# Optimization experiments

Hardware: AMD Instinct MI355X
Metric: run time of the kernel (lower is better)

## Reference

```python
import jax, jax.numpy as jnp
import numpy as np

MI_N, DIS_N = 16384, 8192
EM = 128
E_MM, E_DD = MI_N * 32, DIS_N * 32


def _add_self_loops(edges, ew, n):
    loop = jnp.arange(n, dtype=edges.dtype)
    row = jnp.concatenate([edges[0], loop])
    col = jnp.concatenate([edges[1], loop])
    ew = jnp.concatenate([ew, jnp.ones((n,), ew.dtype)])
    return row, col, ew


def gcn_conv(x, edges, w, b, n, ew=None):
    # PyG GCNConv: symmetric gcn_norm with self-loops (fill 1.0), then
    # out[col] += norm * (x @ w)[row], plus bias.
    if ew is None:
        ew = jnp.ones((edges.shape[1],), x.dtype)
    row, col, ew = _add_self_loops(edges, ew, n)
    deg = jax.ops.segment_sum(ew, col, num_segments=n)
    dinv = jnp.where(deg > 0, jax.lax.rsqrt(deg), 0.0)
    norm = dinv[row] * ew * dinv[col]          # [E+n]
    h = x @ w                                   # [n, d]
    return jax.ops.segment_sum(h[row] * norm[:, None], col, num_segments=n) + b


def gat_conv(x, edges, w, a_src, a_dst, b, n):
    # PyG GATConv, heads=1: per-edge attention LeakyReLU(0.2) + softmax over
    # incoming edges of each target node (self-loops added).
    h = x @ w                                   # [n, d]
    row, col, _ = _add_self_loops(edges, jnp.ones((edges.shape[1],), x.dtype), n)
    e = jax.nn.leaky_relu((h @ a_src)[row] + (h @ a_dst)[col], negative_slope=0.2)
    m = jax.ops.segment_max(e, col, num_segments=n)
    ex = jnp.exp(e - m[col])
    s = jax.ops.segment_sum(ex, col, num_segments=n)
    alpha = ex / s[col]                         # [E+n]
    return jax.ops.segment_sum(h[row] * alpha[:, None], col, num_segments=n) + b


def setup_inputs() -> dict:
    key = jax.random.key(0)
    ks = jax.random.split(key, 24)
    sc = 1.0 / np.sqrt(EM)
    d = {
        'mm_x0': jax.random.normal(ks[0], (MI_N, EM), jnp.float32),
        'dd_x0': jax.random.normal(ks[1], (DIS_N, EM), jnp.float32),
        'w1_mm': jax.random.normal(ks[2], (EM, EM), jnp.float32) * sc,
        'b1_mm': jnp.zeros((EM,), jnp.float32),
        'w2_mm': jax.random.normal(ks[3], (EM, EM), jnp.float32) * sc,
        'b2_mm': jnp.zeros((EM,), jnp.float32),
        'w3_mm': jax.random.normal(ks[4], (EM, EM), jnp.float32) * sc,
        'asrc_mm': jax.random.normal(ks[5], (EM,), jnp.float32) * sc,
        'adst_mm': jax.random.normal(ks[6], (EM,), jnp.float32) * sc,
        'b3_mm': jnp.zeros((EM,), jnp.float32),
        'w1_dd': jax.random.normal(ks[7], (EM, EM), jnp.float32) * sc,
        'b1_dd': jnp.zeros((EM,), jnp.float32),
        'w2_dd': jax.random.normal(ks[8], (EM, EM), jnp.float32) * sc,
        'b2_dd': jnp.zeros((EM,), jnp.float32),
        'w3_dd': jax.random.normal(ks[9], (EM, EM), jnp.float32) * sc,
        'asrc_dd': jax.random.normal(ks[10], (EM,), jnp.float32) * sc,
        'adst_dd': jax.random.normal(ks[11], (EM,), jnp.float32) * sc,
        'b3_dd': jnp.zeros((EM,), jnp.float32),
        'mm_ew': jax.random.uniform(ks[12], (E_MM,), jnp.float32),
        'dd_ew': jax.random.uniform(ks[13], (E_DD,), jnp.float32),
        'mm_edges': jax.random.randint(ks[14], (2, E_MM), 0, MI_N, jnp.int32),
        'dd_edges': jax.random.randint(ks[15], (2, E_DD), 0, DIS_N, jnp.int32),
    }
    return d


def reference(mm_x0, dd_x0, w1_mm, b1_mm, w2_mm, b2_mm, w3_mm, asrc_mm, adst_mm,
              b3_mm, w1_dd, b1_dd, w2_dd, b2_dd, w3_dd, asrc_dd, adst_dd, b3_dd,
              mm_ew, dd_ew, mm_edges, dd_edges):
    elu = jax.nn.elu
    m1 = elu(gcn_conv(mm_x0, mm_edges, w1_mm, b1_mm, MI_N, mm_ew))
    m2 = elu(gcn_conv(m1, mm_edges, w2_mm, b2_mm, MI_N))
    m3 = elu(gat_conv(m2, mm_edges, w3_mm, asrc_mm, adst_mm, b3_mm, MI_N))
    d1 = elu(gcn_conv(dd_x0, dd_edges, w1_dd, b1_dd, DIS_N, dd_ew))
    d2 = elu(gcn_conv(d1, dd_edges, w2_dd, b2_dd, DIS_N))
    d3 = elu(gat_conv(d2, dd_edges, w3_dd, asrc_dd, adst_dd, b3_dd, DIS_N))
    mi_fea = (m1 + m2 + m3) / 3.0
    dis_fea = (d1 + d2 + d3) / 3.0
    score_raw = mi_fea @ dis_fea.T              # [MI_N, DIS_N]
    mn, mx = jnp.min(score_raw), jnp.max(score_raw)
    denom = jnp.where(mx > mn, mx - mn, jnp.asarray(1.0, score_raw.dtype))
    score_norm = jnp.where(mx > mn, (score_raw - mn) / denom,
                           jnp.zeros_like(score_raw))
    score_norm = jnp.clip(score_norm, 0.0, 1.0)
    return score_norm, mi_fea, dis_fea
```

## Files before the change

### kernel.cpp

```cpp
#include <hip/hip_runtime.h>
#include <cstdint>
#include <cstddef>

#define MI_NN 16384
#define DIS_NN 8192
#define EMB 128
#define EMM (MI_NN*32)
#define EDD (DIS_NN*32)

typedef __attribute__((ext_vector_type(8))) short short8;
typedef __attribute__((ext_vector_type(4))) float f32x4;

__device__ __forceinline__ float leakyr(float x){ return x > 0.f ? x : 0.2f*x; }
__device__ __forceinline__ float eluf(float x){ return x > 0.f ? x : expm1f(x); }

__device__ __forceinline__ unsigned bf16u(float x){
  unsigned u = __float_as_uint(x);
  return (u + 0x7FFFu + ((u >> 16) & 1u)) >> 16;
}
__device__ __forceinline__ float bfl(unsigned p){ return __uint_as_float(p << 16); }
__device__ __forceinline__ float bfh(unsigned p){ return __uint_as_float(p & 0xFFFF0000u); }

__global__ __launch_bounds__(256) void k_count2g(const int* __restrict__ c0, int* __restrict__ n0c,
                                                 int E0, int nb0,
                                                 const int* __restrict__ c1, int* __restrict__ n1c,
                                                 int E1, unsigned* __restrict__ ctr){
  if (blockIdx.x == 0 && threadIdx.x == 0) ctr[0] = 0u;
  int b = blockIdx.x;
  const int* col; int* cnt; int E; int t;
  if (b < nb0){ col = c0; cnt = n0c; E = E0; t = b*256 + threadIdx.x; }
  else        { col = c1; cnt = n1c; E = E1; t = (b - nb0)*256 + threadIdx.x; }
  if (t < E) atomicAdd(&cnt[col[t]], 1);
}

__global__ __launch_bounds__(1024) void k_scan2g(const int* __restrict__ cnt0, int* __restrict__ rp0,
                                                 int n0, int E0,
                                                 const int* __restrict__ cnt1, int* __restrict__ rp1,
                                                 int n1, int E1){
  const int* cnt = blockIdx.x ? cnt1 : cnt0;
  int* rowptr    = blockIdx.x ? rp1  : rp0;
  int n          = blockIdx.x ? n1   : n0;
  int E          = blockIdx.x ? E1   : E0;
  __shared__ int lds[1024];
  int t = threadIdx.x;
  int chunk = n >> 10;
  int base = t*chunk;
  int s = 0;
  for (int i = 0; i < chunk; ++i) s += cnt[base+i];
  lds[t] = s; __syncthreads();
  for (int off = 1; off < 1024; off <<= 1){
    int v = (t >= off) ? lds[t-off] : 0;
    __syncthreads();
    lds[t] += v;
    __syncthreads();
  }
  int run = lds[t] - s;
  for (int i = 0; i < chunk; ++i){ rowptr[base+i] = run; run += cnt[base+i]; }
  if (t == 0) rowptr[n] = E;
}

__global__ __launch_bounds__(256) void k_fill2g(
    const int* __restrict__ r0a, const int* __restrict__ c0a, const float* __restrict__ w0a,
    const int* __restrict__ rp0, int* __restrict__ f0, int2* __restrict__ e0,
    int E0, int nb0,
    const int* __restrict__ r1a, const int* __restrict__ c1a, const float* __restrict__ w1a,
    const int* __restrict__ rp1, int* __restrict__ f1, int2* __restrict__ e1,
    int E1){
  int b = blockIdx.x;
  const int *row, *col; const float* ew; const int* rowptr;
  int* fill; int2* epk; int E, t;
  if (b < nb0){ row=r0a; col=c0a; ew=w0a; rowptr=rp0; fill=f0; epk=e0; E=E0; t=b*256+threadIdx.x; }
  else        { row=r1a; col=c1a; ew=w1a; rowptr=rp1; fill=f1; epk=e1; E=E1; t=(b-nb0)*256+threadIdx.x; }
  if (t < E){
    int c = col[t];
    int p = rowptr[c] + atomicAdd(&fill[c], 1);
    epk[p] = make_int2(row[t], __float_as_int(ew[t]));
  }
}

template<int FUSE>
__global__ __launch_bounds__(256) void k_gemm2g(
    const float* __restrict__ X0, const float* __restrict__ W0, ushort* __restrict__ H0, int nb0,
    const float* __restrict__ X1, const float* __restrict__ W1, ushort* __restrict__ H1,
    const float* __restrict__ as0, const float* __restrict__ ad0,
    float* __restrict__ es0, float* __restrict__ ed0,
    const float* __restrict__ as1, const float* __restrict__ ad1,
    float* __restrict__ es1, float* __restrict__ ed1){
  int b = blockIdx.x;
  const float *X, *W, *asr, *ads; ushort* H; float *es, *ed; int rb;
  if (b < nb0){ X=X0; W=W0; H=H0; asr=as0; ads=ad0; es=es0; ed=ed0; rb = b; }
  else        { X=X1; W=W1; H=H1; asr=as1; ads=ad1; es=es1; ed=ed1; rb = b - nb0; }
  __shared__ float wl[EMB*EMB];
  int t = threadIdx.x;
  {
    const float4* W4 = (const float4*)W;
    float4* L4 = (float4*)wl;
    #pragma unroll
    for (int i = 0; i < 16; ++i) L4[t + 256*i] = W4[t + 256*i];
  }
  __syncthreads();
  int jg = t & 31;
  int rg = t >> 5;
  int r0 = rb*32 + rg*4;
  f32x4 acc0 = {0,0,0,0}, acc1 = {0,0,0,0}, acc2 = {0,0,0,0}, acc3 = {0,0,0,0};
  const float4* X4 = (const float4*)X;
  for (int k4 = 0; k4 < 32; ++k4){
    float4 x0 = X4[(size_t)(r0+0)*32 + k4];
    float4 x1 = X4[(size_t)(r0+1)*32 + k4];
    float4 x2 = X4[(size_t)(r0+2)*32 + k4];
    float4 x3 = X4[(size_t)(r0+3)*32 + k4];
#define GSTEP(c0,c1,c2,c3,kq) { f32x4 w4 = *(const f32x4*)&wl[(kq)*EMB + jg*4]; \
      acc0 += (c0)*w4; acc1 += (c1)*w4; acc2 += (c2)*w4; acc3 += (c3)*w4; }
    GSTEP(x0.x, x1.x, x2.x, x3.x, k4*4+0)
    GSTEP(x0.y, x1.y, x2.y, x3.y, k4*4+1)
    GSTEP(x0.z, x1.z, x2.z, x3.z, k4*4+2)
    GSTEP(x0.w, x1.w, x2.w, x3.w, k4*4+3)
#undef GSTEP
  }
#define PACK2(o, a) { o.x = bf16u(a[0]) | (bf16u(a[1])<<16); o.y = bf16u(a[2]) | (bf16u(a[3])<<16); }
  uint2 o0, o1, o2, o3;
  PACK2(o0, acc0) PACK2(o1, acc1) PACK2(o2, acc2) PACK2(o3, acc3)
#undef PACK2
  ushort* out = H + (size_t)r0*EMB + jg*4;
  *(uint2*)(out)         = o0;
  *(uint2*)(out + EMB)   = o1;
  *(uint2*)(out + 2*EMB) = o2;
  *(uint2*)(out + 3*EMB) = o3;

  if (FUSE){
    f32x4 s4 = *(const f32x4*)&asr[jg*4];
    f32x4 d4 = *(const f32x4*)&ads[jg*4];
    float ps0 = acc0[0]*s4[0] + acc0[1]*s4[1] + acc0[2]*s4[2] + acc0[3]*s4[3];
    float ps1 = acc1[0]*s4[0] + acc1[1]*s4[1] + acc1[2]*s4[2] + acc1[3]*s4[3];
    float ps2 = acc2[0]*s4[0] + acc2[1]*s4[1] + acc2[2]*s4[2] + acc2[3]*s4[3];
    float ps3 = acc3[0]*s4[0] + acc3[1]*s4[1] + acc3[2]*s4[2] + acc3[3]*s4[3];
    float pd0 = acc0[0]*d4[0] + acc0[1]*d4[1] + acc0[2]*d4[2] + acc0[3]*d4[3];
    float pd1 = acc1[0]*d4[0] + acc1[1]*d4[1] + acc1[2]*d4[2] + acc1[3]*d4[3];
    float pd2 = acc2[0]*d4[0] + acc2[1]*d4[1] + acc2[2]*d4[2] + acc2[3]*d4[3];
    float pd3 = acc3[0]*d4[0] + acc3[1]*d4[1] + acc3[2]*d4[2] + acc3[3]*d4[3];
    #pragma unroll
    for (int off = 16; off; off >>= 1){
      ps0 += __shfl_xor(ps0, off); ps1 += __shfl_xor(ps1, off);
      ps2 += __shfl_xor(ps2, off); ps3 += __shfl_xor(ps3, off);
      pd0 += __shfl_xor(pd0, off); pd1 += __shfl_xor(pd1, off);
      pd2 += __shfl_xor(pd2, off); pd3 += __shfl_xor(pd3, off);
    }
    if (jg == 0){
      es[r0+0] = ps0; es[r0+1] = ps1; es[r0+2] = ps2; es[r0+3] = ps3;
      ed[r0+0] = pd0; ed[r0+1] = pd1; ed[r0+2] = pd2; ed[r0+3] = pd3;
    }
  }
}

__global__ __launch_bounds__(256) void k_deg2g(
    const int* __restrict__ rp0, const int2* __restrict__ ep0,
    float* __restrict__ d10, float* __restrict__ d20, int n0, int nb0,
    const int* __restrict__ rp1, const int2* __restrict__ ep1,
    float* __restrict__ d11, float* __restrict__ d21, int n1){
  int b = blockIdx.x;
  const int* rowptr; const int2* epk; float *d1, *d2; int n, wid;
  int lane = threadIdx.x & 63;
  if (b < nb0){ rowptr=rp0; epk=ep0; d1=d10; d2=d20; n=n0; wid = (b*256 + threadIdx.x) >> 6; }
  else        { rowptr=rp1; epk=ep1; d1=d11; d2=d21; n=n1; wid = ((b-nb0)*256 + threadIdx.x) >> 6; }
  if (wid >= n) return;
  int beg = rowptr[wid], end = rowptr[wid+1];
  float s = 0.f;
  for (int i = beg + lane; i < end; i += 64) s += __int_as_float(epk[i].y);
  #pragma unroll
  for (int off = 32; off; off >>= 1) s += __shfl_xor(s, off);
  if (lane == 0){
    d1[wid] = rsqrtf(1.0f + s);
    d2[wid] = rsqrtf(1.0f + (float)(end - beg));
  }
}

__global__ __launch_bounds__(256) void k_agg2g(
    const ushort* __restrict__ H0, const float* __restrict__ di0, const int* __restrict__ rp0,
    const int2* __restrict__ ep0, const float* __restrict__ bi0,
    float* __restrict__ xn0, float* __restrict__ fe0, int n0, int nb0,
    const ushort* __restrict__ H1, const float* __restrict__ di1, const int* __restrict__ rp1,
    const int2* __restrict__ ep1, const float* __restrict__ bi1,
    float* __restrict__ xn1, float* __restrict__ fe1, int n1,
    int useew, int femode){
  int b = blockIdx.x;
  const ushort* H; const float* dinv; const int* rowptr; const int2* epk;
  const float* bias; float* xnext; float* fea; int n, wid;
  int lane = threadIdx.x & 63;
  if (b < nb0){ H=H0; dinv=di0; rowptr=rp0; epk=ep0; bias=bi0; xnext=xn0; fea=fe0; n=n0;
                wid = (b*256 + threadIdx.x) >> 6; }
  else        { H=H1; dinv=di1; rowptr=rp1; epk=ep1; bias=bi1; xnext=xn1; fea=fe1; n=n1;
                wid = ((b-nb0)*256 + threadIdx.x) >> 6; }
  if (wid >= n) return;
  int v = wid;
  int half = lane >> 5;
  int hl   = lane & 31;
  float dv = dinv[v];
  uint2 hv = *(const uint2*)(H + (size_t)v*EMB + hl*4);
  float a0, a1, a2, a3;
  if (half == 0){
    a0 = dv*bfl(hv.x); a1 = dv*bfh(hv.x); a2 = dv*bfl(hv.y); a3 = dv*bfh(hv.y);
  } else { a0 = a1 = a2 = a3 = 0.f; }
  int beg = rowptr[v], end = rowptr[v+1];
  int i = beg + half;
  for (; i + 2 < end; i += 4){
    int2 eA = epk[i], eB = epk[i+2];
    float nA = dinv[eA.x], nB = dinv[eB.x];
    if (useew){ nA *= __int_as_float(eA.y); nB *= __int_as_float(eB.y); }
    uint2 hA = *(const uint2*)(H + (size_t)eA.x*EMB + hl*4);
    uint2 hB = *(const uint2*)(H + (size_t)eB.x*EMB + hl*4);
    a0 += nA*bfl(hA.x) + nB*bfl(hB.x);
    a1 += nA*bfh(hA.x) + nB*bfh(hB.x);
    a2 += nA*bfl(hA.y) + nB*bfl(hB.y);
    a3 += nA*bfh(hA.y) + nB*bfh(hB.y);
  }
  if (i < end){
    int2 e = epk[i];
    float nm = dinv[e.x];
    if (useew) nm *= __int_as_float(e.y);
    uint2 h = *(const uint2*)(H + (size_t)e.x*EMB + hl*4);
    a0 += nm*bfl(h.x); a1 += nm*bfh(h.x); a2 += nm*bfl(h.y); a3 += nm*bfh(h.y);
  }
  a0 += __shfl_xor(a0, 32); a1 += __shfl_xor(a1, 32);
  a2 += __shfl_xor(a2, 32); a3 += __shfl_xor(a3, 32);
  if (half == 0){
    float4 b4 = *(const float4*)(bias + hl*4);
    float o0 = eluf(dv*a0 + b4.x), o1 = eluf(dv*a1 + b4.y);
    float o2 = eluf(dv*a2 + b4.z), o3 = eluf(dv*a3 + b4.w);
    *(float4*)(xnext + (size_t)v*EMB + hl*4) = make_float4(o0, o1, o2, o3);
    float* fp = fea + (size_t)v*EMB + hl*4;
    if (femode == 0){
      *(float4*)fp = make_float4(o0, o1, o2, o3);
    } else {
      float4 f = *(float4*)fp;
      *(float4*)fp = make_float4(f.x + o0, f.y + o1, f.z + o2, f.w + o3);
    }
  }
}

__global__ __launch_bounds__(256) void k_gat2g(
    const ushort* __restrict__ H0, const float* __restrict__ es0, const float* __restrict__ ed0,
    const int* __restrict__ rp0, const int2* __restrict__ ep0, const float* __restrict__ bi0,
    float* __restrict__ fe0, unsigned* __restrict__ sh0, int n0, int nb0,
    const ushort* __restrict__ H1, const float* __restrict__ es1, const float* __restrict__ ed1,
    const int* __restrict__ rp1, const int2* __restrict__ ep1, const float* __restrict__ bi1,
    float* __restrict__ fe1, unsigned* __restrict__ sh1, int n1){
  int b = blockIdx.x;
  const ushort* H; const float *es, *ed; const int* rowptr; const int2* epk; const float* bias;
  float* fea; unsigned* shadow; int n, wid;
  int lane = threadIdx.x & 63;
  if (b < nb0){ H=H0; es=es0; ed=ed0; rowptr=rp0; epk=ep0; bias=bi0; fea=fe0; shadow=sh0; n=n0;
                wid = (b*256 + threadIdx.x) >> 6; }
  else        { H=H1; es=es1; ed=ed1; rowptr=rp1; epk=ep1; bias=bi1; fea=fe1; shadow=sh1; n=n1;
                wid = ((b-nb0)*256 + threadIdx.x) >> 6; }
  if (wid >= n) return;
  int v = wid;
  float edv = ed[v];
  float self_e = leakyr(es[v] + edv);
  int beg = rowptr[v], end = rowptr[v+1];
  float m = -3.4e38f, s = 0.f;
  for (int i = beg + lane; i < end; i += 64){
    float e = leakyr(es[epk[i].x] + edv);
    if (e > m){ s = s*expf(m - e) + 1.0f; m = e; }
    else s += expf(e - m);
  }
  #pragma unroll
  for (int off = 32; off; off >>= 1){
    float m2 = __shfl_xor(m, off), s2 = __shfl_xor(s, off);
    float mn_ = fmaxf(m, m2);
    s = s*expf(m - mn_) + s2*expf(m2 - mn_);
    m = mn_;
  }
  {
    float mn_ = fmaxf(m, self_e);
    s = s*expf(m - mn_) + expf(self_e - mn_);
    m = mn_;
  }
  float inv_s = 1.0f / s;
  int half = lane >> 5;
  int hl   = lane & 31;
  uint2 hv = *(const uint2*)(H + (size_t)v*EMB + hl*4);
  float aw = expf(self_e - m)*inv_s;
  float a0, a1, a2, a3;
  if (half == 0){
    a0 = aw*bfl(hv.x); a1 = aw*bfh(hv.x); a2 = aw*bfl(hv.y); a3 = aw*bfh(hv.y);
  } else { a0 = a1 = a2 = a3 = 0.f; }
  int i = beg + half;
  for (; i + 2 < end; i += 4){
    int rA = epk[i].x, rB = epk[i+2].x;
    float aA = expf(leakyr(es[rA] + edv) - m)*inv_s;
    float aB = expf(leakyr(es[rB] + edv) - m)*inv_s;
    uint2 hA = *(const uint2*)(H + (size_t)rA*EMB + hl*4);
    uint2 hB = *(const uint2*)(H + (size_t)rB*EMB + hl*4);
    a0 += aA*bfl(hA.x) + aB*bfl(hB.x);
    a1 += aA*bfh(hA.x) + aB*bfh(hB.x);
    a2 += aA*bfl(hA.y) + aB*bfl(hB.y);
    a3 += aA*bfh(hA.y) + aB*bfh(hB.y);
  }
  if (i < end){
    int r = epk[i].x;
    float a = expf(leakyr(es[r] + edv) - m)*inv_s;
    uint2 h = *(const uint2*)(H + (size_t)r*EMB + hl*4);
    a0 += a*bfl(h.x); a1 += a*bfh(h.x); a2 += a*bfl(h.y); a3 += a*bfh(h.y);
  }
  a0 += __shfl_xor(a0, 32); a1 += __shfl_xor(a1, 32);
  a2 += __shfl_xor(a2, 32); a3 += __shfl_xor(a3, 32);
  if (half == 0){
    float4 b4 = *(const float4*)(bias + hl*4);
    float o0 = eluf(a0 + b4.x), o1 = eluf(a1 + b4.y);
    float o2 = eluf(a2 + b4.z), o3 = eluf(a3 + b4.w);
    float* fp = fea + (size_t)v*EMB + hl*4;
    float4 f = *(float4*)fp;
    float f0 = (f.x + o0)/3.0f, f1 = (f.y + o1)/3.0f;
    float f2 = (f.z + o2)/3.0f, f3 = (f.w + o3)/3.0f;
    *(float4*)fp = make_float4(f0, f1, f2, f3);
    uint2 sh;
    sh.x = bf16u(f0) | (bf16u(f1) << 16);
    sh.y = bf16u(f2) | (bf16u(f3) << 16);
    *(uint2*)(shadow + (size_t)v*64 + hl*2) = sh;
  }
}

__device__ __forceinline__ void stage128(const uint8_t* G, uint8_t* L, int w, int lane){
  #pragma unroll
  for (int c = 0; c < 8; ++c){
    int linear = w*8192 + c*1024 + lane*16;
    int row = linear >> 8, col = linear & 255;
    const void* src = G + row*256 + (col ^ ((row & 7) << 4));
    __builtin_amdgcn_global_load_lds(
        (const __attribute__((address_space(1))) void*)src,
        (__attribute__((address_space(3))) void*)(L + w*8192 + c*1024),
        16, 0, 0);
  }
}

#define NT 16
template<int STORE>
__global__ __launch_bounds__(256) void k_score5(const ushort* __restrict__ Abf,
                                                const ushort* __restrict__ Bbf,
                                                float* __restrict__ S,
                                                float* __restrict__ mmpart){
  __shared__ __align__(16) uint8_t L0[32768];
  __shared__ __align__(16) uint8_t L1[32768];
  __shared__ float red[16];
  __shared__ unsigned sdone;
  const int t = threadIdx.x;
  const int lane = t & 63;
  const int w = t >> 6;
  const int wr = w >> 1, wc = w & 1;
  const int lr = lane & 15, lk = lane >> 4;
  const int i0b = blockIdx.y * 128;
  const int jbase = blockIdx.x * NT;

  stage128((const uint8_t*)(Abf + (size_t)i0b*EMB), L0, w, lane);
  stage128((const uint8_t*)(Bbf + (size_t)jbase*128*EMB), L1, w, lane);
  __syncthreads();

  short8 af[4][4];
  #pragma unroll
  for (int at = 0; at < 4; ++at){
    int ra = wr*64 + at*16 + lr;
    #pragma unroll
    for (int k0 = 0; k0 < 4; ++k0){
      int kb = k0*64 + lk*16;
      af[at][k0] = *(const short8*)&L0[ra*256 + (kb ^ ((ra & 7) << 4))];
    }
  }
  __syncthreads();
  stage128((const uint8_t*)(Bbf + (size_t)(jbase+1)*128*EMB), L0, w, lane);

  float mn = 0.f, sc = 0.f;
  if (STORE){
    mn = mmpart[0];
    float mx = mmpart[1];
    sc = (mx > mn) ? 1.0f/(mx - mn) : 0.0f;
  }
  float lmin = 3.4e38f, lmax = -3.4e38f;

  for (int jt = 0; jt < NT; ++jt){
    uint8_t* curB = (jt & 1) ? L0 : L1;
    f32x4 acc[4][4];
    #pragma unroll
    for (int a = 0; a < 4; ++a)
      #pragma unroll
      for (int b = 0; b < 4; ++b) acc[a][b] = (f32x4){0.f,0.f,0.f,0.f};

    #pragma unroll
    for (int k0 = 0; k0 < 4; ++k0){
      int kb = k0*64 + lk*16;
      short8 bfr[4];
      #pragma unroll
      for (int ct = 0; ct < 4; ++ct){
        int rb = wc*64 + ct*16 + lr;
        bfr[ct] = *(const short8*)&curB[rb*256 + (kb ^ ((rb & 7) << 4))];
      }
      #pragma unroll
      for (int at = 0; at < 4; ++at)
        #pragma unroll
        for (int ct = 0; ct < 4; ++ct)
          acc[at][ct] = __builtin_amdgcn_mfma_f32_16x16x32_bf16(af[at][k0], bfr[ct], acc[at][ct], 0, 0, 0);
    }

    int j0 = (jbase + jt)*128;
    if (STORE){
      #pragma unroll
      for (int at = 0; at < 4; ++at){
        #pragma unroll
        for (int ct = 0; ct < 4; ++ct){
          int colj = j0 + wc*64 + ct*16 + lr;
          int row0 = i0b + wr*64 + at*16 + lk*4;
          #pragma unroll
          for (int q = 0; q < 4; ++q){
            float vv = fminf(fmaxf((acc[at][ct][q] - mn)*sc, 0.f), 1.f);
            S[(size_t)(row0+q)*DIS_NN + colj] = vv;
          }
        }
      }
    } else {
      #pragma unroll
      for (int at = 0; at < 4; ++at)
        #pragma unroll
        for (int ct = 0; ct < 4; ++ct)
          #pragma unroll
          for (int q = 0; q < 4; ++q){
            float vv = acc[at][ct][q];
            lmin = fminf(lmin, vv); lmax = fmaxf(lmax, vv);
          }
    }
    __syncthreads();
    if (jt + 2 < NT)
      stage128((const uint8_t*)(Bbf + (size_t)(jbase+jt+2)*128*EMB), curB, w, lane);
  }

  if (!STORE){
    #pragma unroll
    for (int off = 32; off; off >>= 1){
      lmin = fminf(lmin, __shfl_xor(lmin, off));
      lmax = fmaxf(lmax, __shfl_xor(lmax, off));
    }
    if (lane == 0){ red[w*2] = lmin; red[w*2+1] = lmax; }
    __syncthreads();
    unsigned* ctr = (unsigned*)(mmpart + 1088);
    if (t == 0){
      float a = fminf(fminf(red[0], red[2]), fminf(red[4], red[6]));
      float b = fmaxf(fmaxf(red[1], red[3]), fmaxf(red[5], red[7]));
      int bid = blockIdx.y * 4 + blockIdx.x;
      mmpart[2 + bid*2]     = a;
      mmpart[2 + bid*2 + 1] = b;
      __threadfence();
      sdone = atomicAdd(ctr, 1u);
    }
    __syncthreads();
    if (sdone == 511u){
      __threadfence();
      float mnv = fminf(mmpart[2 + 2*t], mmpart[2 + 2*(t+256)]);
      float mxv = fmaxf(mmpart[3 + 2*t], mmpart[3 + 2*(t+256)]);
      #pragma unroll
      for (int off = 32; off; off >>= 1){
        mnv = fminf(mnv, __shfl_xor(mnv, off));
        mxv = fmaxf(mxv, __shfl_xor(mxv, off));
      }
      if (lane == 0){ red[w*2] = mnv; red[w*2+1] = mxv; }
      __syncthreads();
      if (t == 0){
        float a = fminf(fminf(red[0], red[2]), fminf(red[4], red[6]));
        float b = fmaxf(fmaxf(red[1], red[3]), fmaxf(red[5], red[7]));
        mmpart[0] = a; mmpart[1] = b;
      }
    }
  }
}

extern "C" void kernel_launch(void* const* d_in, const int* in_sizes, int n_in,
                              void* d_out, int out_size, void* d_ws, size_t ws_size,
                              hipStream_t stream){
  (void)in_sizes; (void)n_in; (void)out_size; (void)ws_size;
  const float* mm_x0  = (const float*)d_in[0];
  const float* dd_x0  = (const float*)d_in[1];
  const float* w1_mm  = (const float*)d_in[2];
  const float* b1_mm  = (const float*)d_in[3];
  const float* w2_mm  = (const float*)d_in[4];
  const float* b2_mm  = (const float*)d_in[5];
  const float* w3_mm  = (const float*)d_in[6];
  const float* asrc_mm= (const float*)d_in[7];
  const float* adst_mm= (const float*)d_in[8];
  const float* b3_mm  = (const float*)d_in[9];
  const float* w1_dd  = (const float*)d_in[10];
  const float* b1_dd  = (const float*)d_in[11];
  const float* w2_dd  = (const float*)d_in[12];
  const float* b2_dd  = (const float*)d_in[13];
  const float* w3_dd  = (const float*)d_in[14];
  const float* asrc_dd= (const float*)d_in[15];
  const float* adst_dd= (const float*)d_in[16];
  const float* b3_dd  = (const float*)d_in[17];
  const float* mm_ew  = (const float*)d_in[18];
  const float* dd_ew  = (const float*)d_in[19];
  const int* mm_edges = (const int*)d_in[20];
  const int* dd_edges = (const int*)d_in[21];

  float* S = (float*)d_out;
  float* p = S;
  float* A0m = p;  p += (size_t)MI_NN*EMB;
  float* A1m = p;  p += (size_t)MI_NN*EMB;
  float* A0d = p;  p += (size_t)DIS_NN*EMB;
  float* A1d = p;  p += (size_t)DIS_NN*EMB;
  ushort* Hbm = (ushort*)p; p += (size_t)MI_NN*EMB/2;
  ushort* Hbd = (ushort*)p; p += (size_t)DIS_NN*EMB/2;
  float* DEG1m = p; p += MI_NN;
  float* DEG2m = p; p += MI_NN;
  float* ESm   = p; p += MI_NN;
  float* EDm   = p; p += MI_NN;
  float* DEG1d = p; p += DIS_NN;
  float* DEG2d = p; p += DIS_NN;
  float* ESd   = p; p += DIS_NN;
  float* EDd   = p; p += DIS_NN;
  int* CNTm  = (int*)p; p += MI_NN;
  int* CNTd  = (int*)p; p += DIS_NN;
  int* FILLm = (int*)p; p += MI_NN;
  int* FILLd = (int*)p; p += DIS_NN;
  int* RPm   = (int*)p; p += MI_NN + 64;
  int* RPd   = (int*)p; p += DIS_NN + 64;
  int2* EPKm = (int2*)p; p += (size_t)EMM*2;
  int2* EPKd = (int2*)p; p += (size_t)EDD*2;
  float* FEA_MI  = S + (size_t)MI_NN * DIS_NN;
  float* FEA_DIS = FEA_MI + (size_t)MI_NN*EMB;

  float* MM = (float*)d_ws;
  ushort* Abf = (ushort*)((char*)d_ws + 16384);
  ushort* Bbf = Abf + (size_t)MI_NN * EMB;

  const int* erow_m = mm_edges;
  const int* ecol_m = mm_edges + EMM;
  const int* erow_d = dd_edges;
  const int* ecol_d = dd_edges + EDD;

  hipMemsetAsync(CNTm, 0, (size_t)2*(MI_NN + DIS_NN)*sizeof(int), stream);
  k_count2g<<<EMM/256 + EDD/256, 256, 0, stream>>>(ecol_m, CNTm, EMM, EMM/256,
                                                   ecol_d, CNTd, EDD,
                                                   (unsigned*)(MM + 1088));
  k_scan2g<<<2, 1024, 0, stream>>>(CNTm, RPm, MI_NN, EMM, CNTd, RPd, DIS_NN, EDD);
  k_fill2g<<<EMM/256 + EDD/256, 256, 0, stream>>>(erow_m, ecol_m, mm_ew, RPm, FILLm, EPKm,
                                                  EMM, EMM/256,
                                                  erow_d, ecol_d, dd_ew, RPd, FILLd, EPKd,
                                                  EDD);
  const int GB = MI_NN/32 + DIS_NN/32;
  const int AB = MI_NN/4 + DIS_NN/4;
  k_gemm2g<0><<<GB, 256, 0, stream>>>(mm_x0, w1_mm, Hbm, MI_NN/32, dd_x0, w1_dd, Hbd,
                                      nullptr, nullptr, nullptr, nullptr,
                                      nullptr, nullptr, nullptr, nullptr);
  k_deg2g<<<AB, 256, 0, stream>>>(RPm, EPKm, DEG1m, DEG2m, MI_NN, MI_NN/4,
                                  RPd, EPKd, DEG1d, DEG2d, DIS_NN);
  k_agg2g<<<AB, 256, 0, stream>>>(Hbm, DEG1m, RPm, EPKm, b1_mm, A0m, FEA_MI, MI_NN, MI_NN/4,
                                  Hbd, DEG1d, RPd, EPKd, b1_dd, A0d, FEA_DIS, DIS_NN, 1, 0);
  k_gemm2g<0><<<GB, 256, 0, stream>>>(A0m, w2_mm, Hbm, MI_NN/32, A0d, w2_dd, Hbd,
                                      nullptr, nullptr, nullptr, nullptr,
                                      nullptr, nullptr, nullptr, nullptr);
  k_agg2g<<<AB, 256, 0, stream>>>(Hbm, DEG2m, RPm, EPKm, b2_mm, A1m, FEA_MI, MI_NN, MI_NN/4,
                                  Hbd, DEG2d, RPd, EPKd, b2_dd, A1d, FEA_DIS, DIS_NN, 0, 1);
  k_gemm2g<1><<<GB, 256, 0, stream>>>(A1m, w3_mm, Hbm, MI_NN/32, A1d, w3_dd, Hbd,
                                      asrc_mm, adst_mm, ESm, EDm,
                                      asrc_dd, adst_dd, ESd, EDd);
  k_gat2g<<<AB, 256, 0, stream>>>(Hbm, ESm, EDm, RPm, EPKm, b3_mm, FEA_MI, (unsigned*)Abf, MI_NN, MI_NN/4,
                                  Hbd, ESd, EDd, RPd, EPKd, b3_dd, FEA_DIS, (unsigned*)Bbf, DIS_NN);
  k_score5<0><<<dim3(DIS_NN/(128*NT), MI_NN/128), 256, 0, stream>>>(Abf, Bbf, nullptr, MM);
  k_score5<1><<<dim3(DIS_NN/(128*NT), MI_NN/128), 256, 0, stream>>>(Abf, Bbf, S, MM);
}
```

Measured before the change: 437.3 us.

## Move layer GEMMs to bf16 MFMA with bf16 activations and wider gather unroll

Adds a prep kernel that converts the input features to bf16 and the six weight matrices to transposed bf16. The three per-layer FP32 FMA GEMMs are replaced by an MFMA 16x16x32 bf16 kernel on 128-row tiles, staged into LDS with swizzled global_load_lds. Intermediate activations are now written as bf16 instead of fp32, halving GEMM input traffic. The GCN and GAT edge-gather loops are unrolled from 2 to 4 edges per step. Rounding the GEMM inputs to bf16 adds precision loss, and the prep kernel adds a launch.

Result: faster. 396.5 us (-9.3%).

```diff
diff --git a/kernel.cpp b/kernel.cpp
--- a/kernel.cpp
+++ b/kernel.cpp
@@ -20,6 +20,35 @@
 }
 __device__ __forceinline__ float bfl(unsigned p){ return __uint_as_float(p << 16); }
 __device__ __forceinline__ float bfh(unsigned p){ return __uint_as_float(p & 0xFFFF0000u); }
+
+__global__ __launch_bounds__(256) void k_prep(const float* __restrict__ x0m, const float* __restrict__ x0d,
+    const float* __restrict__ w1m, const float* __restrict__ w2m, const float* __restrict__ w3m,
+    const float* __restrict__ w1d, const float* __restrict__ w2d, const float* __restrict__ w3d,
+    ushort* __restrict__ Xm, ushort* __restrict__ Xd, ushort* __restrict__ Wt){
+  int b = blockIdx.x, t = threadIdx.x;
+  if (b < 1536){
+    const float* src; ushort* dst; int i;
+    if (b < 1024){ src = x0m; dst = Xm; i = b*256 + t; }
+    else         { src = x0d; dst = Xd; i = (b-1024)*256 + t; }
+    const float4* X4 = (const float4*)src;
+    float4 a = X4[(size_t)i*2], c = X4[(size_t)i*2+1];
+    union { ushort u[8]; uint4 v; } r;
+    r.u[0]=(ushort)bf16u(a.x); r.u[1]=(ushort)bf16u(a.y);
+    r.u[2]=(ushort)bf16u(a.z); r.u[3]=(ushort)bf16u(a.w);
+    r.u[4]=(ushort)bf16u(c.x); r.u[5]=(ushort)bf16u(c.y);
+    r.u[6]=(ushort)bf16u(c.z); r.u[7]=(ushort)bf16u(c.w);
+    ((uint4*)dst)[i] = r.v;
+  } else {
+    int m = b - 1536;
+    const float* W = (m==0)?w1m:(m==1)?w2m:(m==2)?w3m:(m==3)?w1d:(m==4)?w2d:w3d;
+    ushort* dst = Wt + m*16384;
+    for (int it = 0; it < 64; ++it){
+      int o = it*256 + t;
+      int j = o >> 7, k = o & 127;
+      dst[o] = (ushort)bf16u(W[k*128 + j]);
+    }
+  }
+}
 
 __global__ __launch_bounds__(256) void k_count2g(const int* __restrict__ c0, int* __restrict__ n0c,
                                                  int E0, int nb0,
@@ -78,77 +107,112 @@
   }
 }
 
+__device__ __forceinline__ void stage128(const uint8_t* G, uint8_t* L, int w, int lane){
+  #pragma unroll
+  for (int c = 0; c < 8; ++c){
+    int linear = w*8192 + c*1024 + lane*16;
+    int row = linear >> 8, col = linear & 255;
+    const void* src = G + row*256 + (col ^ ((row & 7) << 4));
+    __builtin_amdgcn_global_load_lds(
+        (const __attribute__((address_space(1))) void*)src,
+        (__attribute__((address_space(3))) void*)(L + w*8192 + c*1024),
+        16, 0, 0);
+  }
+}
+
 template<int FUSE>
-__global__ __launch_bounds__(256) void k_gemm2g(
-    const float* __restrict__ X0, const float* __restrict__ W0, ushort* __restrict__ H0, int nb0,
-    const float* __restrict__ X1, const float* __restrict__ W1, ushort* __restrict__ H1,
+__global__ __launch_bounds__(256) void k_gemm_mfma(
+    const ushort* __restrict__ X0, const ushort* __restrict__ Wt0, ushort* __restrict__ H0, int nb0,
+    const ushort* __restrict__ X1, const ushort* __restrict__ Wt1, ushort* __restrict__ H1,
     const float* __restrict__ as0, const float* __restrict__ ad0,
     float* __restrict__ es0, float* __restrict__ ed0,
     const float* __restrict__ as1, const float* __restrict__ ad1,
     float* __restrict__ es1, float* __restrict__ ed1){
+  __shared__ __align__(16) uint8_t Xl[32768];
+  __shared__ __align__(16) uint8_t Wl[32768];
+  __shared__ float esp[2][128], edp[2][128];
   int b = blockIdx.x;
-  const float *X, *W, *asr, *ads; ushort* H; float *es, *ed; int rb;
-  if (b < nb0){ X=X0; W=W0; H=H0; asr=as0; ads=ad0; es=es0; ed=ed0; rb = b; }
-  else        { X=X1; W=W1; H=H1; asr=as1; ads=ad1; es=es1; ed=ed1; rb = b - nb0; }
-  __shared__ float wl[EMB*EMB];
-  int t = threadIdx.x;
-  {
-    const float4* W4 = (const float4*)W;
-    float4* L4 = (float4*)wl;
-    #pragma unroll
-    for (int i = 0; i < 16; ++i) L4[t + 256*i] = W4[t + 256*i];
-  }
+  const ushort *X, *Wt; ushort* H; const float *asr, *ads; float *es, *ed; int rb;
+  if (b < nb0){ X=X0; Wt=Wt0; H=H0; asr=as0; ads=ad0; es=es0; ed=ed0; rb = b; }
+  else        { X=X1; Wt=Wt1; H=H1; asr=as1; ads=ad1; es=es1; ed=ed1; rb = b - nb0; }
+  const int t = threadIdx.x;
+  const int lane = t & 63, w = t >> 6;
+  const int wr = w >> 1, wc = w & 1;
+  const int lr = lane & 15, lk = lane >> 4;
+  const int i0 = rb*128;
+
+  stage128((const uint8_t*)(X + (size_t)i0*EMB), Xl, w, lane);
+  stage128((const uint8_t*)Wt, Wl, w, lane);
   __syncthreads();
-  int jg = t & 31;
-  int rg = t >> 5;
-  int r0 = rb*32 + rg*4;
-  f32x4 acc0 = {0,0,0,0}, acc1 = {0,0,0,0}, acc2 = {0,0,0,0}, acc3 = {0,0,0,0};
-  const float4* X4 = (const float4*)X;
-  for (int k4 = 0; k4 < 32; ++k4){
-    float4 x0 = X4[(size_t)(r0+0)*32 + k4];
-    float4 x1 = X4[(size_t)(r0+1)*32 + k4];
-    float4 x2 = X4[(size_t)(r0+2)*32 + k4];
-    float4 x3 = X4[(size_t)(r0+3)*32 + k4];
-#define GSTEP(c0,c1,c2,c3,kq) { f32x4 w4 = *(const f32x4*)&wl[(kq)*EMB + jg*4]; \
-      acc0 += (c0)*w4; acc1 += (c1)*w4; acc2 += (c2)*w4; acc3 += (c3)*w4; }
-    GSTEP(x0.x, x1.x, x2.x, x3.x, k4*4+0)
-    GSTEP(x0.y, x1.y, x2.y, x3.y, k4*4+1)
-    GSTEP(x0.z, x1.z, x2.z, x3.z, k4*4+2)
-    GSTEP(x0.w, x1.w, x2.w, x3.w, k4*4+3)
-#undef GSTEP
-  }
-#define PACK2(o, a) { o.x = bf16u(a[0]) | (bf16u(a[1])<<16); o.y = bf16u(a[2]) | (bf16u(a[3])<<16); }
-  uint2 o0, o1, o2, o3;
-  PACK2(o0, acc0) PACK2(o1, acc1) PACK2(o2, acc2) PACK2(o3, acc3)
-#undef PACK2
-  ushort* out = H + (size_t)r0*EMB + jg*4;
-  *(uint2*)(out)         = o0;
-  *(uint2*)(out + EMB)   = o1;
-  *(uint2*)(out + 2*EMB) = o2;
-  *(uint2*)(out + 3*EMB) = o3;
-
+
+  short8 af[4][4];
+  #pragma unroll
+  for (int at = 0; at < 4; ++at){
+    int ra = wr*64 + at*16 + lr;
+    #pragma unroll
+    for (int k0 = 0; k0 < 4; ++k0){
+      int kb = k0*64 + lk*16;
+      af[at][k0] = *(const short8*)&Xl[ra*256 + (kb ^ ((ra & 7) << 4))];
+    }
+  }
+  f32x4 acc[4][4];
+  #pragma unroll
+  for (int a = 0; a < 4; ++a)
+    #pragma unroll
+    for (int c = 0; c < 4; ++c) acc[a][c] = (f32x4){0.f,0.f,0.f,0.f};
+  #pragma unroll
+  for (int k0 = 0; k0 < 4; ++k0){
+    int kb = k0*64 + lk*16;
+    short8 bfr[4];
+    #pragma unroll
+    for (int ct = 0; ct < 4; ++ct){
+      int rbw = wc*64 + ct*16 + lr;
+      bfr[ct] = *(const short8*)&Wl[rbw*256 + (kb ^ ((rbw & 7) << 4))];
+    }
+    #pragma unroll
+    for (int at = 0; at < 4; ++at)
+      #pragma unroll
+      for (int ct = 0; ct < 4; ++ct)
+        acc[at][ct] = __builtin_amdgcn_mfma_f32_16x16x32_bf16(af[at][k0], bfr[ct], acc[at][ct], 0, 0, 0);
+  }
+  #pragma unroll
+  for (int at = 0; at < 4; ++at){
+    #pragma unroll
+    for (int ct = 0; ct < 4; ++ct){
+      int colj = wc*64 + ct*16 + lr;
+      int row0 = i0 + wr*64 + at*16 + lk*4;
+      #pragma unroll
+      for (int q = 0; q < 4; ++q)
+        H[(size_t)(row0+q)*EMB + colj] = (ushort)bf16u(acc[at][ct][q]);
+    }
+  }
   if (FUSE){
-    f32x4 s4 = *(const f32x4*)&asr[jg*4];
-    f32x4 d4 = *(const f32x4*)&ads[jg*4];
-    float ps0 = acc0[0]*s4[0] + acc0[1]*s4[1] + acc0[2]*s4[2] + acc0[3]*s4[3];
-    float ps1 = acc1[0]*s4[0] + acc1[1]*s4[1] + acc1[2]*s4[2] + acc1[3]*s4[3];
-    float ps2 = acc2[0]*s4[0] + acc2[1]*s4[1] + acc2[2]*s4[2] + acc2[3]*s4[3];
-    float ps3 = acc3[0]*s4[0] + acc3[1]*s4[1] + acc3[2]*s4[2] + acc3[3]*s4[3];
-    float pd0 = acc0[0]*d4[0] + acc0[1]*d4[1] + acc0[2]*d4[2] + acc0[3]*d4[3];
-    float pd1 = acc1[0]*d4[0] + acc1[1]*d4[1] + acc1[2]*d4[2] + acc1[3]*d4[3];
-    float pd2 = acc2[0]*d4[0] + acc2[1]*d4[1] + acc2[2]*d4[2] + acc2[3]*d4[3];
-    float pd3 = acc3[0]*d4[0] + acc3[1]*d4[1] + acc3[2]*d4[2] + acc3[3]*d4[3];
-    #pragma unroll
-    for (int off = 16; off; off >>= 1){
-      ps0 += __shfl_xor(ps0, off); ps1 += __shfl_xor(ps1, off);
-      ps2 += __shfl_xor(ps2, off); ps3 += __shfl_xor(ps3, off);
-      pd0 += __shfl_xor(pd0, off); pd1 += __shfl_xor(pd1, off);
-      pd2 += __shfl_xor(pd2, off); pd3 += __shfl_xor(pd3, off);
-    }
-    if (jg == 0){
-      es[r0+0] = ps0; es[r0+1] = ps1; es[r0+2] = ps2; es[r0+3] = ps3;
-      ed[r0+0] = pd0; ed[r0+1] = pd1; ed[r0+2] = pd2; ed[r0+3] = pd3;
-    }
+    float sv[4], dv4[4];
+    #pragma unroll
+    for (int ct = 0; ct < 4; ++ct){
+      sv[ct]  = asr[wc*64 + ct*16 + lr];
+      dv4[ct] = ads[wc*64 + ct*16 + lr];
+    }
+    #pragma unroll
+    for (int at = 0; at < 4; ++at){
+      #pragma unroll
+      for (int q = 0; q < 4; ++q){
+        float ps = acc[at][0][q]*sv[0] + acc[at][1][q]*sv[1] + acc[at][2][q]*sv[2] + acc[at][3][q]*sv[3];
+        float pd = acc[at][0][q]*dv4[0] + acc[at][1][q]*dv4[1] + acc[at][2][q]*dv4[2] + acc[at][3][q]*dv4[3];
+        #pragma unroll
+        for (int off = 8; off; off >>= 1){
+          ps += __shfl_xor(ps, off);
+          pd += __shfl_xor(pd, off);
+        }
+        if (lr == 0){
+          int rl = wr*64 + at*16 + lk*4 + q;
+          esp[wc][rl] = ps; edp[wc][rl] = pd;
+        }
+      }
+    }
+    __syncthreads();
+    if (t < 128) es[i0 + t] = esp[0][t] + esp[1][t];
+    else { int r = t - 128; ed[i0 + r] = edp[0][r] + edp[1][r]; }
   }
 }
 
@@ -177,14 +241,14 @@
 __global__ __launch_bounds__(256) void k_agg2g(
     const ushort* __restrict__ H0, const float* __restrict__ di0, const int* __restrict__ rp0,
     const int2* __restrict__ ep0, const float* __restrict__ bi0,
-    float* __restrict__ xn0, float* __restrict__ fe0, int n0, int nb0,
+    ushort* __restrict__ xn0, float* __restrict__ fe0, int n0, int nb0,
     const ushort* __restrict__ H1, const float* __restrict__ di1, const int* __restrict__ rp1,
     const int2* __restrict__ ep1, const float* __restrict__ bi1,
-    float* __restrict__ xn1, float* __restrict__ fe1, int n1,
+    ushort* __restrict__ xn1, float* __restrict__ fe1, int n1,
     int useew, int femode){
   int b = blockIdx.x;
   const ushort* H; const float* dinv; const int* rowptr; const int2* epk;
-  const float* bias; float* xnext; float* fea; int n, wid;
+  const float* bias; ushort* xnext; float* fea; int n, wid;
   int lane = threadIdx.x & 63;
   if (b < nb0){ H=H0; dinv=di0; rowptr=rp0; epk=ep0; bias=bi0; xnext=xn0; fea=fe0; n=n0;
                 wid = (b*256 + threadIdx.x) >> 6; }
@@ -202,18 +266,21 @@
   } else { a0 = a1 = a2 = a3 = 0.f; }
   int beg = rowptr[v], end = rowptr[v+1];
   int i = beg + half;
-  for (; i + 2 < end; i += 4){
-    int2 eA = epk[i], eB = epk[i+2];
-    float nA = dinv[eA.x], nB = dinv[eB.x];
-    if (useew){ nA *= __int_as_float(eA.y); nB *= __int_as_float(eB.y); }
+  for (; i + 6 < end; i += 8){
+    int2 eA = epk[i], eB = epk[i+2], eC = epk[i+4], eD = epk[i+6];
+    float nA = dinv[eA.x], nB = dinv[eB.x], nC = dinv[eC.x], nD = dinv[eD.x];
+    if (useew){ nA *= __int_as_float(eA.y); nB *= __int_as_float(eB.y);
+                nC *= __int_as_float(eC.y); nD *= __int_as_float(eD.y); }
     uint2 hA = *(const uint2*)(H + (size_t)eA.x*EMB + hl*4);
     uint2 hB = *(const uint2*)(H + (size_t)eB.x*EMB + hl*4);
-    a0 += nA*bfl(hA.x) + nB*bfl(hB.x);
-    a1 += nA*bfh(hA.x) + nB*bfh(hB.x);
-    a2 += nA*bfl(hA.y) + nB*bfl(hB.y);
-    a3 += nA*bfh(hA.y) + nB*bfh(hB.y);
-  }
-  if (i < end){
+    uint2 hC = *(const uint2*)(H + (size_t)eC.x*EMB + hl*4);
+    uint2 hD = *(const uint2*)(H + (size_t)eD.x*EMB + hl*4);
+    a0 += nA*bfl(hA.x) + nB*bfl(hB.x) + nC*bfl(hC.x) + nD*bfl(hD.x);
+    a1 += nA*bfh(hA.x) + nB*bfh(hB.x) + nC*bfh(hC.x) + nD*bfh(hD.x);
+    a2 += nA*bfl(hA.y) + nB*bfl(hB.y) + nC*bfl(hC.y) + nD*bfl(hD.y);
+    a3 += nA*bfh(hA.y) + nB*bfh(hB.y) + nC*bfh(hC.y) + nD*bfh(hD.y);
+  }
+  for (; i < end; i += 2){
     int2 e = epk[i];
     float nm = dinv[e.x];
     if (useew) nm *= __int_as_float(e.y);
@@ -226,7 +293,10 @@
     float4 b4 = *(const float4*)(bias + hl*4);
     float o0 = eluf(dv*a0 + b4.x), o1 = eluf(dv*a1 + b4.y);
     float o2 = eluf(dv*a2 + b4.z), o3 = eluf(dv*a3 + b4.w);
-    *(float4*)(xnext + (size_t)v*EMB + hl*4) = make_float4(o0, o1, o2, o3);
+    uint2 xn2;
+    xn2.x = bf16u(o0) | (bf16u(o1) << 16);
+    xn2.y = bf16u(o2) | (bf16u(o3) << 16);
+    *(uint2*)(xnext + (size_t)v*EMB + hl*4) = xn2;
     float* fp = fea + (size_t)v*EMB + hl*4;
     if (femode == 0){
       *(float4*)fp = make_float4(o0, o1, o2, o3);
@@ -285,18 +355,22 @@
     a0 = aw*bfl(hv.x); a1 = aw*bfh(hv.x); a2 = aw*bfl(hv.y); a3 = aw*bfh(hv.y);
   } else { a0 = a1 = a2 = a3 = 0.f; }
   int i = beg + half;
-  for (; i + 2 < end; i += 4){
-    int rA = epk[i].x, rB = epk[i+2].x;
+  for (; i + 6 < end; i += 8){
+    int rA = epk[i].x, rB = epk[i+2].x, rC = epk[i+4].x, rD = epk[i+6].x;
     float aA = expf(leakyr(es[rA] + edv) - m)*inv_s;
     float aB = expf(leakyr(es[rB] + edv) - m)*inv_s;
+    float aC = expf(leakyr(es[rC] + edv) - m)*inv_s;
+    float aD = expf(leakyr(es[rD] + edv) - m)*inv_s;
     uint2 hA = *(const uint2*)(H + (size_t)rA*EMB + hl*4);
     uint2 hB = *(const uint2*)(H + (size_t)rB*EMB + hl*4);
-    a0 += aA*bfl(hA.x) + aB*bfl(hB.x);
-    a1 += aA*bfh(hA.x) + aB*bfh(hB.x);
-    a2 += aA*bfl(hA.y) + aB*bfl(hB.y);
-    a3 += aA*bfh(hA.y) + aB*bfh(hB.y);
-  }
-  if (i < end){
+    uint2 hC = *(const uint2*)(H + (size_t)rC*EMB + hl*4);
+    uint2 hD = *(const uint2*)(H + (size_t)rD*EMB + hl*4);
+    a0 += aA*bfl(hA.x) + aB*bfl(hB.x) + aC*bfl(hC.x) + aD*bfl(hD.x);
+    a1 += aA*bfh(hA.x) + aB*bfh(hB.x) + aC*bfh(hC.x) + aD*bfh(hD.x);
+    a2 += aA*bfl(hA.y) + aB*bfl(hB.y) + aC*bfl(hC.y) + aD*bfl(hD.y);
+    a3 += aA*bfh(hA.y) + aB*bfh(hB.y) + aC*bfh(hC.y) + aD*bfh(hD.y);
+  }
+  for (; i < end; i += 2){
     int r = epk[i].x;
     float a = expf(leakyr(es[r] + edv) - m)*inv_s;
     uint2 h = *(const uint2*)(H + (size_t)r*EMB + hl*4);
@@ -317,19 +391,6 @@
     sh.x = bf16u(f0) | (bf16u(f1) << 16);
     sh.y = bf16u(f2) | (bf16u(f3) << 16);
     *(uint2*)(shadow + (size_t)v*64 + hl*2) = sh;
-  }
-}
-
-__device__ __forceinline__ void stage128(const uint8_t* G, uint8_t* L, int w, int lane){
-  #pragma unroll
-  for (int c = 0; c < 8; ++c){
-    int linear = w*8192 + c*1024 + lane*16;
-    int row = linear >> 8, col = linear & 255;
-    const void* src = G + row*256 + (col ^ ((row & 7) << 4));
-    __builtin_amdgcn_global_load_lds(
-        (const __attribute__((address_space(1))) void*)src,
-        (__attribute__((address_space(3))) void*)(L + w*8192 + c*1024),
-        16, 0, 0);
   }
 }
 
@@ -499,12 +560,11 @@
 
   float* S = (float*)d_out;
   float* p = S;
-  float* A0m = p;  p += (size_t)MI_NN*EMB;
-  float* A1m = p;  p += (size_t)MI_NN*EMB;
-  float* A0d = p;  p += (size_t)DIS_NN*EMB;
-  float* A1d = p;  p += (size_t)DIS_NN*EMB;
+  ushort* Xm  = (ushort*)p; p += (size_t)MI_NN*EMB/2;
+  ushort* Xd  = (ushort*)p; p += (size_t)DIS_NN*EMB/2;
   ushort* Hbm = (ushort*)p; p += (size_t)MI_NN*EMB/2;
   ushort* Hbd = (ushort*)p; p += (size_t)DIS_NN*EMB/2;
+  ushort* WT  = (ushort*)p; p += 6*16384/2;
   float* DEG1m = p; p += MI_NN;
   float* DEG2m = p; p += MI_NN;
   float* ESm   = p; p += MI_NN;
@@ -533,6 +593,8 @@
   const int* erow_d = dd_edges;
   const int* ecol_d = dd_edges + EDD;
 
+  k_prep<<<1542, 256, 0, stream>>>(mm_x0, dd_x0, w1_mm, w2_mm, w3_mm,
+                                   w1_dd, w2_dd, w3_dd, Xm, Xd, WT);
   hipMemsetAsync(CNTm, 0, (size_t)2*(MI_NN + DIS_NN)*sizeof(int), stream);
   k_count2g<<<EMM/256 + EDD/256, 256, 0, stream>>>(ecol_m, CNTm, EMM, EMM/256,
                                                    ecol_d, CNTd, EDD,
@@ -542,23 +604,26 @@
                                                   EMM, EMM/256,
                                                   erow_d, ecol_d, dd_ew, RPd, FILLd, EPKd,
                                                   EDD);
-  const int GB = MI_NN/32 + DIS_NN/32;
+  const int GB = MI_NN/128 + DIS_NN/128;
   const int AB = MI_NN/4 + DIS_NN/4;
-  k_gemm2g<0><<<GB, 256, 0, stream>>>(mm_x0, w1_mm, Hbm, MI_NN/32, dd_x0, w1_dd, Hbd,
-                                      nullptr, nullptr, nullptr, nullptr,
-                                      nullptr, nullptr, nullptr, nullptr);
+  k_gemm_mfma<0><<<GB, 256, 0, stream>>>(Xm, WT + 0*16384, Hbm, MI_NN/128,
+                                         Xd, WT + 3*16384, Hbd,
+                                         nullptr, nullptr, nullptr, nullptr,
+                                         nullptr, nullptr, nullptr, nullptr);
   k_deg2g<<<AB, 256, 0, stream>>>(RPm, EPKm, DEG1m, DEG2m, MI_NN, MI_NN/4,
                                   RPd, EPKd, DEG1d, DEG2d, DIS_NN);
-  k_agg2g<<<AB, 256, 0, stream>>>(Hbm, DEG1m, RPm, EPKm, b1_mm, A0m, FEA_MI, MI_NN, MI_NN/4,
-                                  Hbd, DEG1d, RPd, EPKd, b1_dd, A0d, FEA_DIS, DIS_NN, 1, 0);
-  k_gemm2g<0><<<GB, 256, 0, stream>>>(A0m, w2_mm, Hbm, MI_NN/32, A0d, w2_dd, Hbd,
-                                      nullptr, nullptr, nullptr, nullptr,
-                                      nullptr, nullptr, nullptr, nullptr);
-  k_agg2g<<<AB, 256, 0, stream>>>(Hbm, DEG2m, RPm, EPKm, b2_mm, A1m, FEA_MI, MI_NN, MI_NN/4,
-                                  Hbd, DEG2d, RPd, EPKd, b2_dd, A1d, FEA_DIS, DIS_NN, 0, 1);
-  k_gemm2g<1><<<GB, 256, 0, stream>>>(A1m, w3_mm, Hbm, MI_NN/32, A1d, w3_dd, Hbd,
-                                      asrc_mm, adst_mm, ESm, EDm,
-                                      asrc_dd, adst_dd, ESd, EDd);
+  k_agg2g<<<AB, 256, 0, stream>>>(Hbm, DEG1m, RPm, EPKm, b1_mm, Xm, FEA_MI, MI_NN, MI_NN/4,
+                                  Hbd, DEG1d, RPd, EPKd, b1_dd, Xd, FEA_DIS, DIS_NN, 1, 0);
+  k_gemm_mfma<0><<<GB, 256, 0, stream>>>(Xm, WT + 1*16384, Hbm, MI_NN/128,
+                                         Xd, WT + 4*16384, Hbd,
+                                         nullptr, nullptr, nullptr, nullptr,
+                                         nullptr, nullptr, nullptr, nullptr);
+  k_agg2g<<<AB, 256, 0, stream>>>(Hbm, DEG2m, RPm, EPKm, b2_mm, Xm, FEA_MI, MI_NN, MI_NN/4,
+                                  Hbd, DEG2d, RPd, EPKd, b2_dd, Xd, FEA_DIS, DIS_NN, 0, 1);
+  k_gemm_mfma<1><<<GB, 256, 0, stream>>>(Xm, WT + 2*16384, Hbm, MI_NN/128,
+                                         Xd, WT + 5*16384, Hbd,
+                                         asrc_mm, adst_mm, ESm, EDm,
+                                         asrc_dd, adst_dd, ESd, EDd);
   k_gat2g<<<AB, 256, 0, stream>>>(Hbm, ESm, EDm, RPm, EPKm, b3_mm, FEA_MI, (unsigned*)Abf, MI_NN, MI_NN/4,
                                   Hbd, ESd, EDd, RPd, EPKd, b3_dd, FEA_DIS, (unsigned*)Bbf, DIS_NN);
   k_score5<0><<<dim3(DIS_NN/(128*NT), MI_NN/128), 256, 0, stream>>>(Abf, Bbf, nullptr, MM);
```
